# Optimization experiments

Hardware: AMD Instinct MI355X
Metric: run time of the kernel (lower is better)

Reference implementation:

```python
import jax, jax.numpy as jnp
import numpy as np

N, S, K, H, D = 8192, 16384, 16, 8, 512
E = N * K
HEAD_DIM = D // H


def setup_inputs() -> dict:
    key = jax.random.key(0)
    ks = jax.random.split(key, 12)
    x = jax.random.normal(ks[0], (N, D), jnp.float32)
    # every destination row gets K edges so softmax rows are never empty
    row_index = jnp.repeat(jnp.arange(N, dtype=jnp.int32), K)  # [E], sorted
    src_index = jax.random.randint(ks[1], (E,), 0, S, dtype=jnp.int32)
    att_bias = jax.random.normal(ks[2], (H, E), jnp.float32)
    dist = jax.random.uniform(ks[3], (E,), jnp.float32, minval=0.5, maxval=10.0)
    pos = jax.random.normal(ks[4], (N, 3), jnp.float32)
    src_pos = jax.random.normal(ks[5], (S, 3), jnp.float32)
    org_to_src = jax.random.randint(ks[6], (S,), 0, N, dtype=jnp.int32)
    scale = 1.0 / np.sqrt(D).astype(np.float32)
    Wq = jax.random.normal(ks[7], (D, D), jnp.float32) * scale
    bq = jax.random.normal(ks[8], (D,), jnp.float32) * 0.01
    Wk = jax.random.normal(ks[9], (D, D), jnp.float32) * scale
    bk = jax.random.normal(ks[10], (D,), jnp.float32) * 0.01
    return {"x": x, "row_index": row_index, "src_index": src_index,
            "att_bias": att_bias, "dist": dist, "pos": pos, "src_pos": src_pos,
            "org_to_src": org_to_src, "Wq": Wq, "bq": bq, "Wk": Wk, "bk": bk}


def reference(x, row_index, src_index, att_bias, dist, pos, src_pos, org_to_src,
              Wq, bq, Wk, bk):
    n, d_model = x.shape
    h, e = att_bias.shape
    hd = d_model // h
    # Projections -> [N, H, hd]; key gathered to the source list via org_to_src -> [S, H, hd]
    q = (x @ Wq + bq).reshape(n, h, hd)
    k_src = ((x @ Wk + bk).reshape(n, h, hd))[org_to_src]
    # Per-edge masked logits: (q/sqrt(hd)) . k + att_bias   (COO sparse attention)
    q_e = q[row_index]                       # [E, H, hd]
    k_e = k_src[src_index]                   # [E, H, hd]
    logits = jnp.einsum('ehd,ehd->eh', q_e, k_e) / np.sqrt(hd).astype(np.float32)
    logits = logits + att_bias.T             # [E, H]
    # Segment softmax over edges sharing a destination row
    m = jax.ops.segment_max(logits, row_index, num_segments=n)      # [N, H]
    p = jnp.exp(logits - m[row_index])
    z = jax.ops.segment_sum(p, row_index, num_segments=n)           # [N, H]
    att = p / z[row_index]                                          # [E, H]
    # Distance reweighting: 1/dist with dist==0 -> 0 weight
    safe = jnp.where(dist == 0, 1.0, dist)
    inv_d = jnp.where(dist == 0, 0.0, 1.0 / safe)
    att = att * inv_d[:, None]
    # dst_vec = att @ src_pos ; src_vec = (att @ 1) * pos   (both as segment sums)
    dst = jax.ops.segment_sum(att[:, :, None] * src_pos[src_index][:, None, :],
                              row_index, num_segments=n)            # [N, H, 3]
    asum = jax.ops.segment_sum(att, row_index, num_segments=n)      # [N, H]
    feat = dst - asum[:, :, None] * pos[:, None, :]                 # [N, H, 3]
    return feat.reshape(n, h * 3)
```

## Files before the change

kernel.cpp:

```cpp
#include <hip/hip_runtime.h>

#define N_ROWS 8192
#define D_MODEL 512
#define KT 512
#define NC 1024
#define NHEAD 8
#define KEDGE 16
#define NEDGE (N_ROWS * KEDGE)
#define PLANE 256

using f32x4  = __attribute__((ext_vector_type(4))) float;
using bf16x8 = __attribute__((ext_vector_type(8))) __bf16;
using u16x8  = __attribute__((ext_vector_type(8))) unsigned short;

__device__ __forceinline__ unsigned short bf16_rtne(float f) {
    unsigned u = __float_as_uint(f);
    u += 0x7FFFu + ((u >> 16) & 1u);
    return (unsigned short)(u >> 16);
}
__device__ __forceinline__ float from_bf16(unsigned short b) {
    return __uint_as_float(((unsigned)b) << 16);
}

#define GLOAD16(gp, lp) __builtin_amdgcn_global_load_lds( \
    (__attribute__((address_space(1))) void*)(void*)(gp), \
    (__attribute__((address_space(3))) void*)(lp), 16, 0, 0)

__global__ __launch_bounds__(256) void prep(const float* __restrict__ x,
                                            const float* __restrict__ Wq,
                                            const float* __restrict__ Wk,
                                            const int* __restrict__ src_index,
                                            const int* __restrict__ org_to_src,
                                            const float* __restrict__ att_bias,
                                            const float* __restrict__ dist,
                                            const float* __restrict__ src_pos,
                                            unsigned short* __restrict__ Xb,
                                            unsigned short* __restrict__ Bt,
                                            int* __restrict__ KN,
                                            float4* __restrict__ Rec,
                                            float* __restrict__ AtT) {
    if (blockIdx.x < 2048) {
        const int i = (blockIdx.x * 256 + threadIdx.x) * 8;
        const float4 a = *reinterpret_cast<const float4*>(x + i);
        const float4 b = *reinterpret_cast<const float4*>(x + i + 4);
        u16x8 o;
        o[0] = bf16_rtne(a.x); o[1] = bf16_rtne(a.y);
        o[2] = bf16_rtne(a.z); o[3] = bf16_rtne(a.w);
        o[4] = bf16_rtne(b.x); o[5] = bf16_rtne(b.y);
        o[6] = bf16_rtne(b.z); o[7] = bf16_rtne(b.w);
        *reinterpret_cast<u16x8*>(Xb + i) = o;
    } else if (blockIdx.x < 4096) {
        const int gid = (blockIdx.x - 2048) * 256 + threadIdx.x;
        const int j = gid >> 9;
        const int k = gid & 511;
        const float* W = (j < 512) ? Wq : Wk;
        Bt[(size_t)j * KT + k] = bf16_rtne(W[k * D_MODEL + (j & 511)]);
    } else {
        const int ge = (blockIdx.x - 4096) * 256 + threadIdx.x;
        const int s = src_index[ge];
        KN[ge] = org_to_src[s];
        const float d = dist[ge];
        float4 r;
        r.x = src_pos[s * 3 + 0];
        r.y = src_pos[s * 3 + 1];
        r.z = src_pos[s * 3 + 2];
        r.w = (d == 0.f) ? 0.f : 1.f / d;
        Rec[ge] = r;
        float4 b0, b1;
        b0.x = att_bias[0 * (size_t)NEDGE + ge];
        b0.y = att_bias[1 * (size_t)NEDGE + ge];
        b0.z = att_bias[2 * (size_t)NEDGE + ge];
        b0.w = att_bias[3 * (size_t)NEDGE + ge];
        b1.x = att_bias[4 * (size_t)NEDGE + ge];
        b1.y = att_bias[5 * (size_t)NEDGE + ge];
        b1.z = att_bias[6 * (size_t)NEDGE + ge];
        b1.w = att_bias[7 * (size_t)NEDGE + ge];
        *reinterpret_cast<float4*>(AtT + (size_t)ge * 8)     = b0;
        *reinterpret_cast<float4*>(AtT + (size_t)ge * 8 + 4) = b1;
    }
}

__global__ __launch_bounds__(256) void gemm_qk(
    const unsigned short* __restrict__ Xb, const unsigned short* __restrict__ Bt,
    const float* __restrict__ bq, const float* __restrict__ bk,
    unsigned short* __restrict__ QA, unsigned short* __restrict__ QB,
    unsigned short* __restrict__ KA, unsigned short* __restrict__ KB)
{
    __shared__ __align__(16) unsigned short As[128 * 32];
    __shared__ __align__(16) unsigned short Bs[128 * 32];

    const int tid  = threadIdx.x;
    const int lane = tid & 63;
    const int wave = tid >> 6;
    const int wr = wave >> 1, wc = wave & 1;
    const int row0 = blockIdx.x * 128, col0 = blockIdx.y * 128;

    f32x4 acc[4][4];
    #pragma unroll
    for (int m = 0; m < 4; ++m)
        #pragma unroll
        for (int n = 0; n < 4; ++n)
            acc[m][n] = (f32x4){0.f, 0.f, 0.f, 0.f};

    const int strow = tid >> 2;
    const int stcol = (tid & 3) * 8;

    for (int kt = 0; kt < KT / 32; ++kt) {
        const int kb = kt * 32;
        const unsigned short* ga = Xb + (size_t)(row0 + strow) * D_MODEL + kb + stcol;
        const unsigned short* gb = Bt + (size_t)(col0 + strow) * KT + kb + stcol;
        GLOAD16(ga,                 &As[strow * 32 + stcol]);
        GLOAD16(ga + 64 * D_MODEL,  &As[(64 + strow) * 32 + stcol]);
        GLOAD16(gb,                 &Bs[strow * 32 + stcol]);
        GLOAD16(gb + 64 * KT,       &Bs[(64 + strow) * 32 + stcol]);
        __syncthreads();

        bf16x8 afr[4], bfr[4];
        #pragma unroll
        for (int m = 0; m < 4; ++m)
            afr[m] = __builtin_bit_cast(bf16x8, *reinterpret_cast<const u16x8*>(
                &As[(wr * 64 + m * 16 + (lane & 15)) * 32 + (lane >> 4) * 8]));
        #pragma unroll
        for (int n = 0; n < 4; ++n)
            bfr[n] = __builtin_bit_cast(bf16x8, *reinterpret_cast<const u16x8*>(
                &Bs[(wc * 64 + n * 16 + (lane & 15)) * 32 + (lane >> 4) * 8]));

        #pragma unroll
        for (int m = 0; m < 4; ++m)
            #pragma unroll
            for (int n = 0; n < 4; ++n)
                acc[m][n] = __builtin_amdgcn_mfma_f32_16x16x32_bf16(afr[m], bfr[n], acc[m][n], 0, 0, 0);
        __syncthreads();
    }

    #pragma unroll
    for (int m = 0; m < 4; ++m) {
        const int row = row0 + wr * 64 + m * 16 + (lane >> 4) * 4;
        #pragma unroll
        for (int n = 0; n < 4; ++n) {
            const int c = col0 + wc * 64 + n * 16 + (lane & 15);
            const float bias = (c < 512) ? bq[c] : bk[c - 512];
            const int cc = c & 511;
            const int h = cc >> 6, din = cc & 63;
            unsigned short* plane = (c < 512) ? ((din < 32) ? QA : QB)
                                              : ((din < 32) ? KA : KB);
            const int off = h * 32 + (din & 31);
            #pragma unroll
            for (int r = 0; r < 4; ++r)
                plane[(size_t)(row + r) * PLANE + off] = bf16_rtne(acc[m][n][r] + bias);
        }
    }
}

__global__ __launch_bounds__(256) void edge_kernel(
    const unsigned short* __restrict__ QA, const unsigned short* __restrict__ QB,
    const unsigned short* __restrict__ KA, const unsigned short* __restrict__ KB,
    const int* __restrict__ KN,
    const float4* __restrict__ Rec,
    const float* __restrict__ AtT,
    const float* __restrict__ pos,
    float* __restrict__ out)
{
    const int lane = threadIdx.x & 63;
    const int wave = threadIdx.x >> 6;
    const int n = blockIdx.x * 4 + wave;
    const int ll = lane & 31;
    const int half = lane >> 5;
    const int h = ll >> 2;

    const u16x8 qa = *reinterpret_cast<const u16x8*>(QA + (size_t)n * PLANE + ll * 8);
    const u16x8 qb = *reinterpret_cast<const u16x8*>(QB + (size_t)n * PLANE + ll * 8);
    float qaf[8], qbf[8];
    #pragma unroll
    for (int i = 0; i < 8; ++i) { qaf[i] = from_bf16(qa[i]); qbf[i] = from_bf16(qb[i]); }

    int kne[8];
    #pragma unroll
    for (int i = 0; i < 8; ++i) kne[i] = KN[n * KEDGE + 2 * i + half];

    float pA[8];
    #pragma unroll
    for (int i = 0; i < 8; ++i) {
        const u16x8 kv = *reinterpret_cast<const u16x8*>(
            KA + (size_t)kne[i] * PLANE + ll * 8);
        float p = 0.f;
        #pragma unroll
        for (int j = 0; j < 8; ++j) p += qaf[j] * from_bf16(kv[j]);
        pA[i] = p;
    }
    float logit[8];
    #pragma unroll
    for (int i = 0; i < 8; ++i) {
        const u16x8 kv = *reinterpret_cast<const u16x8*>(
            KB + (size_t)kne[i] * PLANE + ll * 8);
        float p = pA[i];
        #pragma unroll
        for (int j = 0; j < 8; ++j) p += qbf[j] * from_bf16(kv[j]);
        p += __shfl_xor(p, 1);
        p += __shfl_xor(p, 2);
        logit[i] = p * 0.125f + AtT[(size_t)(n * KEDGE + 2 * i + half) * 8 + h];
    }

    float mx = logit[0];
    #pragma unroll
    for (int i = 1; i < 8; ++i) mx = fmaxf(mx, logit[i]);
    mx = fmaxf(mx, __shfl_xor(mx, 32));
    float pe[8];
    float z = 0.f;
    #pragma unroll
    for (int i = 0; i < 8; ++i) { pe[i] = __expf(logit[i] - mx); z += pe[i]; }
    z += __shfl_xor(z, 32);
    const float rz = 1.f / z;

    float d0 = 0.f, d1 = 0.f, d2 = 0.f, asum = 0.f;
    #pragma unroll
    for (int i = 0; i < 8; ++i) {
        const float4 r = Rec[n * KEDGE + 2 * i + half];
        const float w = pe[i] * rz * r.w;
        d0 += w * r.x; d1 += w * r.y; d2 += w * r.z;
        asum += w;
    }
    d0 += __shfl_xor(d0, 32);
    d1 += __shfl_xor(d1, 32);
    d2 += __shfl_xor(d2, 32);
    asum += __shfl_xor(asum, 32);

    const int c = ll & 3;
    if (half == 0 && c < 3) {
        const float dc = (c == 0) ? d0 : ((c == 1) ? d1 : d2);
        out[n * 24 + h * 3 + c] = dc - asum * pos[n * 3 + c];
    }
}

extern "C" void kernel_launch(void* const* d_in, const int* in_sizes, int n_in,
                              void* d_out, int out_size, void* d_ws, size_t ws_size,
                              hipStream_t stream) {
    const float* x          = (const float*)d_in[0];
    const int*   src_index  = (const int*)d_in[2];
    const float* att_bias   = (const float*)d_in[3];
    const float* dist       = (const float*)d_in[4];
    const float* pos        = (const float*)d_in[5];
    const float* src_pos    = (const float*)d_in[6];
    const int*   org_to_src = (const int*)d_in[7];
    const float* Wq         = (const float*)d_in[8];
    const float* bq         = (const float*)d_in[9];
    const float* Wk         = (const float*)d_in[10];
    const float* bk         = (const float*)d_in[11];
    float* out = (float*)d_out;

    char* ws = (char*)d_ws;
    unsigned short* Xb  = (unsigned short*)(ws);
    unsigned short* Bt  = (unsigned short*)(ws + ( 8u << 20));
    unsigned short* QA  = (unsigned short*)(ws + ( 9u << 20));
    unsigned short* QB  = (unsigned short*)(ws + (13u << 20));
    unsigned short* KA  = (unsigned short*)(ws + (17u << 20));
    unsigned short* KB  = (unsigned short*)(ws + (21u << 20));
    int*            KN  = (int*)           (ws + (25u << 20));
    float4*         Rec = (float4*)        (ws + (26u << 20));
    float*          AtT = (float*)         (ws + (28u << 20));

    prep<<<dim3(4608), dim3(256), 0, stream>>>(
        x, Wq, Wk, src_index, org_to_src, att_bias, dist, src_pos,
        Xb, Bt, KN, Rec, AtT);
    gemm_qk<<<dim3(N_ROWS / 128, NC / 128), dim3(256), 0, stream>>>(
        Xb, Bt, bq, bk, QA, QB, KA, KB);
    edge_kernel<<<dim3(N_ROWS / 4), dim3(256), 0, stream>>>(
        QA, QB, KA, KB, KN, Rec, AtT, pos, out);
}
```

Baseline: 48.30 us.

## Double-buffer GEMM with swizzled LDS, XCD-aware block mapping, unified Q/K layout

The QK projection GEMM now uses 512 threads, a K-tile of 64, double-buffered LDS with an XOR swizzle, and a 1D grid remapped so that neighbouring row tiles land on the same XCD. The split QA/QB/KA/KB half-planes are replaced with plain row-major Q and K buffers. The edge kernel reads two 16-byte chunks per gathered key row in a single loop instead of two separate passes. The goal is to hide global-to-LDS latency, cut bank conflicts, improve L2 locality, and simplify the gathers, at the cost of more LDS per block and one barrier per tile.

```diff
diff --git a/kernel.cpp b/kernel.cpp
--- a/kernel.cpp
+++ b/kernel.cpp
@@ -7,7 +7,7 @@
 #define NHEAD 8
 #define KEDGE 16
 #define NEDGE (N_ROWS * KEDGE)
-#define PLANE 256
+#define BK 64
 
 using f32x4  = __attribute__((ext_vector_type(4))) float;
 using bf16x8 = __attribute__((ext_vector_type(8))) __bf16;
@@ -80,81 +80,99 @@
     }
 }
 
-__global__ __launch_bounds__(256) void gemm_qk(
+__global__ __launch_bounds__(512) void gemm_qk(
     const unsigned short* __restrict__ Xb, const unsigned short* __restrict__ Bt,
     const float* __restrict__ bq, const float* __restrict__ bk,
-    unsigned short* __restrict__ QA, unsigned short* __restrict__ QB,
-    unsigned short* __restrict__ KA, unsigned short* __restrict__ KB)
+    unsigned short* __restrict__ Qp, unsigned short* __restrict__ Kp)
 {
-    __shared__ __align__(16) unsigned short As[128 * 32];
-    __shared__ __align__(16) unsigned short Bs[128 * 32];
+    __shared__ __align__(16) unsigned short As[2][128 * BK];
+    __shared__ __align__(16) unsigned short Bs[2][128 * BK];
 
     const int tid  = threadIdx.x;
     const int lane = tid & 63;
     const int wave = tid >> 6;
-    const int wr = wave >> 1, wc = wave & 1;
-    const int row0 = blockIdx.x * 128, col0 = blockIdx.y * 128;
-
-    f32x4 acc[4][4];
+    const int wr   = wave >> 2;
+    const int wc   = wave & 3;
+
+    const int bid = blockIdx.x;
+    const int xcd = bid & 7;
+    const int j   = bid >> 3;
+    const int rp  = xcd * 8 + (j >> 3);
+    const int cp  = j & 7;
+    const int row0 = rp * 128, col0 = cp * 128;
+
+    f32x4 acc[4][2];
     #pragma unroll
     for (int m = 0; m < 4; ++m)
         #pragma unroll
-        for (int n = 0; n < 4; ++n)
+        for (int n = 0; n < 2; ++n)
             acc[m][n] = (f32x4){0.f, 0.f, 0.f, 0.f};
 
-    const int strow = tid >> 2;
-    const int stcol = (tid & 3) * 8;
-
-    for (int kt = 0; kt < KT / 32; ++kt) {
-        const int kb = kt * 32;
-        const unsigned short* ga = Xb + (size_t)(row0 + strow) * D_MODEL + kb + stcol;
-        const unsigned short* gb = Bt + (size_t)(col0 + strow) * KT + kb + stcol;
-        GLOAD16(ga,                 &As[strow * 32 + stcol]);
-        GLOAD16(ga + 64 * D_MODEL,  &As[(64 + strow) * 32 + stcol]);
-        GLOAD16(gb,                 &Bs[strow * 32 + stcol]);
-        GLOAD16(gb + 64 * KT,       &Bs[(64 + strow) * 32 + stcol]);
+    const int crow = tid >> 3;
+    const int sc   = ((tid & 7) ^ (crow & 7)) * 8;
+
+    const unsigned short* gA = Xb + (size_t)(row0 + crow) * D_MODEL + sc;
+    const unsigned short* gB = Bt + (size_t)(col0 + crow) * KT     + sc;
+
+    #define STAGE(b, kb) do { \
+        GLOAD16(gA + (kb),                &As[b][tid * 8]); \
+        GLOAD16(gA + (kb) + 64 * D_MODEL, &As[b][(tid + 512) * 8]); \
+        GLOAD16(gB + (kb),                &Bs[b][tid * 8]); \
+        GLOAD16(gB + (kb) + 64 * KT,      &Bs[b][(tid + 512) * 8]); \
+    } while (0)
+
+    STAGE(0, 0);
+    __syncthreads();
+
+    int buf = 0;
+    for (int kt = 0; kt < KT / BK; ++kt) {
+        if (kt < KT / BK - 1) STAGE(buf ^ 1, (kt + 1) * BK);
+        #pragma unroll
+        for (int kk = 0; kk < 2; ++kk) {
+            const int kc = kk * 4 + (lane >> 4);
+            bf16x8 afr[4], bfr[2];
+            #pragma unroll
+            for (int m = 0; m < 4; ++m) {
+                const int r = wr * 64 + m * 16 + (lane & 15);
+                afr[m] = __builtin_bit_cast(bf16x8, *reinterpret_cast<const u16x8*>(
+                    &As[buf][r * BK + ((kc ^ (r & 7)) * 8)]));
+            }
+            #pragma unroll
+            for (int n = 0; n < 2; ++n) {
+                const int r = wc * 32 + n * 16 + (lane & 15);
+                bfr[n] = __builtin_bit_cast(bf16x8, *reinterpret_cast<const u16x8*>(
+                    &Bs[buf][r * BK + ((kc ^ (r & 7)) * 8)]));
+            }
+            #pragma unroll
+            for (int m = 0; m < 4; ++m)
+                #pragma unroll
+                for (int n = 0; n < 2; ++n)
+                    acc[m][n] = __builtin_amdgcn_mfma_f32_16x16x32_bf16(
+                        afr[m], bfr[n], acc[m][n], 0, 0, 0);
+        }
         __syncthreads();
-
-        bf16x8 afr[4], bfr[4];
-        #pragma unroll
-        for (int m = 0; m < 4; ++m)
-            afr[m] = __builtin_bit_cast(bf16x8, *reinterpret_cast<const u16x8*>(
-                &As[(wr * 64 + m * 16 + (lane & 15)) * 32 + (lane >> 4) * 8]));
-        #pragma unroll
-        for (int n = 0; n < 4; ++n)
-            bfr[n] = __builtin_bit_cast(bf16x8, *reinterpret_cast<const u16x8*>(
-                &Bs[(wc * 64 + n * 16 + (lane & 15)) * 32 + (lane >> 4) * 8]));
-
-        #pragma unroll
-        for (int m = 0; m < 4; ++m)
-            #pragma unroll
-            for (int n = 0; n < 4; ++n)
-                acc[m][n] = __builtin_amdgcn_mfma_f32_16x16x32_bf16(afr[m], bfr[n], acc[m][n], 0, 0, 0);
-        __syncthreads();
-    }
+        buf ^= 1;
+    }
+    #undef STAGE
 
     #pragma unroll
     for (int m = 0; m < 4; ++m) {
         const int row = row0 + wr * 64 + m * 16 + (lane >> 4) * 4;
         #pragma unroll
-        for (int n = 0; n < 4; ++n) {
-            const int c = col0 + wc * 64 + n * 16 + (lane & 15);
-            const float bias = (c < 512) ? bq[c] : bk[c - 512];
+        for (int n = 0; n < 2; ++n) {
+            const int c = col0 + wc * 32 + n * 16 + (lane & 15);
             const int cc = c & 511;
-            const int h = cc >> 6, din = cc & 63;
-            unsigned short* plane = (c < 512) ? ((din < 32) ? QA : QB)
-                                              : ((din < 32) ? KA : KB);
-            const int off = h * 32 + (din & 31);
+            unsigned short* plane = (c < 512) ? Qp : Kp;
+            const float bias = (c < 512) ? bq[cc] : bk[cc];
             #pragma unroll
             for (int r = 0; r < 4; ++r)
-                plane[(size_t)(row + r) * PLANE + off] = bf16_rtne(acc[m][n][r] + bias);
+                plane[(size_t)(row + r) * D_MODEL + cc] = bf16_rtne(acc[m][n][r] + bias);
         }
     }
 }
 
 __global__ __launch_bounds__(256) void edge_kernel(
-    const unsigned short* __restrict__ QA, const unsigned short* __restrict__ QB,
-    const unsigned short* __restrict__ KA, const unsigned short* __restrict__ KB,
+    const unsigned short* __restrict__ Qp, const unsigned short* __restrict__ Kp,
     const int* __restrict__ KN,
     const float4* __restrict__ Rec,
     const float* __restrict__ AtT,
@@ -167,35 +185,29 @@
     const int ll = lane & 31;
     const int half = lane >> 5;
     const int h = ll >> 2;
-
-    const u16x8 qa = *reinterpret_cast<const u16x8*>(QA + (size_t)n * PLANE + ll * 8);
-    const u16x8 qb = *reinterpret_cast<const u16x8*>(QB + (size_t)n * PLANE + ll * 8);
-    float qaf[8], qbf[8];
-    #pragma unroll
-    for (int i = 0; i < 8; ++i) { qaf[i] = from_bf16(qa[i]); qbf[i] = from_bf16(qb[i]); }
+    const int o1 = h * 64 + (ll & 3) * 8;
+    const int o2 = o1 + 32;
+
+    const u16x8 q1 = *reinterpret_cast<const u16x8*>(Qp + (size_t)n * D_MODEL + o1);
+    const u16x8 q2 = *reinterpret_cast<const u16x8*>(Qp + (size_t)n * D_MODEL + o2);
+    float qf1[8], qf2[8];
+    #pragma unroll
+    for (int i = 0; i < 8; ++i) { qf1[i] = from_bf16(q1[i]); qf2[i] = from_bf16(q2[i]); }
 
     int kne[8];
     #pragma unroll
     for (int i = 0; i < 8; ++i) kne[i] = KN[n * KEDGE + 2 * i + half];
 
-    float pA[8];
+    float logit[8];
     #pragma unroll
     for (int i = 0; i < 8; ++i) {
-        const u16x8 kv = *reinterpret_cast<const u16x8*>(
-            KA + (size_t)kne[i] * PLANE + ll * 8);
+        const unsigned short* kp = Kp + (size_t)kne[i] * D_MODEL;
+        const u16x8 k1 = *reinterpret_cast<const u16x8*>(kp + o1);
+        const u16x8 k2 = *reinterpret_cast<const u16x8*>(kp + o2);
         float p = 0.f;
         #pragma unroll
-        for (int j = 0; j < 8; ++j) p += qaf[j] * from_bf16(kv[j]);
-        pA[i] = p;
-    }
-    float logit[8];
-    #pragma unroll
-    for (int i = 0; i < 8; ++i) {
-        const u16x8 kv = *reinterpret_cast<const u16x8*>(
-            KB + (size_t)kne[i] * PLANE + ll * 8);
-        float p = pA[i];
-        #pragma unroll
-        for (int j = 0; j < 8; ++j) p += qbf[j] * from_bf16(kv[j]);
+        for (int jj = 0; jj < 8; ++jj)
+            p += qf1[jj] * from_bf16(k1[jj]) + qf2[jj] * from_bf16(k2[jj]);
         p += __shfl_xor(p, 1);
         p += __shfl_xor(p, 2);
         logit[i] = p * 0.125f + AtT[(size_t)(n * KEDGE + 2 * i + half) * 8 + h];
@@ -251,10 +263,8 @@
     char* ws = (char*)d_ws;
     unsigned short* Xb  = (unsigned short*)(ws);
     unsigned short* Bt  = (unsigned short*)(ws + ( 8u << 20));
-    unsigned short* QA  = (unsigned short*)(ws + ( 9u << 20));
-    unsigned short* QB  = (unsigned short*)(ws + (13u << 20));
-    unsigned short* KA  = (unsigned short*)(ws + (17u << 20));
-    unsigned short* KB  = (unsigned short*)(ws + (21u << 20));
+    unsigned short* Qp  = (unsigned short*)(ws + ( 9u << 20));
+    unsigned short* Kp  = (unsigned short*)(ws + (17u << 20));
     int*            KN  = (int*)           (ws + (25u << 20));
     float4*         Rec = (float4*)        (ws + (26u << 20));
     float*          AtT = (float*)         (ws + (28u << 20));
@@ -262,8 +272,7 @@
     prep<<<dim3(4608), dim3(256), 0, stream>>>(
         x, Wq, Wk, src_index, org_to_src, att_bias, dist, src_pos,
         Xb, Bt, KN, Rec, AtT);
-    gemm_qk<<<dim3(N_ROWS / 128, NC / 128), dim3(256), 0, stream>>>(
-        Xb, Bt, bq, bk, QA, QB, KA, KB);
+    gemm_qk<<<dim3(512), dim3(512), 0, stream>>>(Xb, Bt, bq, bk, Qp, Kp);
     edge_kernel<<<dim3(N_ROWS / 4), dim3(256), 0, stream>>>(
-        QA, QB, KA, KB, KN, Rec, AtT, pos, out);
-}
+        Qp, Kp, KN, Rec, AtT, pos, out);
+}
```

After: 44.39 us. 8.1% less time.
